# Performance work log

Hardware: AMD Instinct MI355X
Metric: run time of the kernel (lower is better)

## Reference

```python
import jax, jax.numpy as jnp
import numpy as np

B, S, E, H, LD, P, NC = 4, 256, 256, 8, 128, 256, 2
N = S * P  # total points (static)
EPS = 1e-5


def setup_inputs() -> dict:
    key = jax.random.key(0)
    ks = jax.random.split(key, 12)
    r = lambda i, shape, s: jax.random.normal(ks[i], shape, jnp.float32) * s
    return dict(
        gl_feats=jax.random.normal(ks[0], (S, B, E), jnp.float32),
        lo_feats=jax.random.normal(ks[1], (B, N, LD), jnp.float32),
        centroids=jax.random.normal(ks[2], (B, S, 2), jnp.float32),
        np_cluster=jnp.full((S,), P, jnp.int32),
        fc1_w=r(3, (16, 2), 0.5), fc1_b=jnp.zeros(16, jnp.float32),
        fc2_w=r(4, (E, 16), 0.1), fc2_b=jnp.zeros(E, jnp.float32),
        in_proj_w=r(5, (3 * E, E), 0.05), in_proj_b=jnp.zeros(3 * E, jnp.float32),
        out_proj_w=r(6, (E, E), 0.05), out_proj_b=jnp.zeros(E, jnp.float32),
        conv2_w=r(7, (E // 2, LD + E), 0.05), conv2_b=jnp.zeros(E // 2, jnp.float32),
        bn2_gamma=jnp.ones(E // 2, jnp.float32), bn2_beta=jnp.zeros(E // 2, jnp.float32),
        bn2_mean=jnp.zeros(E // 2, jnp.float32), bn2_var=jnp.ones(E // 2, jnp.float32),
        conv3_w=r(8, (64, E // 2), 0.05), conv3_b=jnp.zeros(64, jnp.float32),
        bn3_gamma=jnp.ones(64, jnp.float32), bn3_beta=jnp.zeros(64, jnp.float32),
        bn3_mean=jnp.zeros(64, jnp.float32), bn3_var=jnp.ones(64, jnp.float32),
        conv4_w=r(9, (NC, 64), 0.05), conv4_b=jnp.zeros(NC, jnp.float32),
    )


def _bn(z, g, b, m, v):
    # inference-mode BatchNorm1d over the channel (last) axis
    return (z - m) * jax.lax.rsqrt(v + EPS) * g + b


def reference(gl_feats, lo_feats, centroids, np_cluster,
              fc1_w, fc1_b, fc2_w, fc2_b,
              in_proj_w, in_proj_b, out_proj_w, out_proj_b,
              conv2_w, conv2_b, bn2_gamma, bn2_beta, bn2_mean, bn2_var,
              conv3_w, conv3_b, bn3_gamma, bn3_beta, bn3_mean, bn3_var,
              conv4_w, conv4_b):
    # positional encoding of centroids: Linear(2,16) -> leaky_relu -> Linear(16,E)
    h = centroids @ fc1_w.T + fc1_b                      # [B,S,16]
    h = jnp.where(h >= 0, h, 0.01 * h)                   # leaky_relu_, slope 0.01
    pos = h @ fc2_w.T + fc2_b                            # [B,S,E]
    x = gl_feats.transpose(1, 0, 2) + pos                # [B,S,E] (torch MHA is seq-first)

    # MultiheadAttention (self-attn, eval-mode dropout=identity)
    qkv = x @ in_proj_w.T + in_proj_b                    # [B,S,3E]
    q, k, v = jnp.split(qkv, 3, axis=-1)
    dh = E // H
    qh = q.reshape(B, S, H, dh)
    kh = k.reshape(B, S, H, dh)
    vh = v.reshape(B, S, H, dh)
    scores = jnp.einsum('bqhd,bkhd->bhqk', qh, kh) * (1.0 / np.sqrt(dh))
    attn = jax.nn.softmax(scores, axis=-1)               # [B,H,S,S]
    ctx = jnp.einsum('bhqk,bkhd->bqhd', attn, vh).reshape(B, S, E)
    attn_out = ctx @ out_proj_w.T + out_proj_b           # [B,S,E]

    # segment-broadcast: replace the python repeat/cat loop with a gather
    cluster_ids = jnp.repeat(jnp.arange(S), np_cluster, total_repeat_length=N)  # [N]
    global_feat = attn_out[:, cluster_ids, :]            # [B,N,E]

    pc = jnp.concatenate([lo_feats, global_feat], axis=2)  # [B,N,LD+E]
    # 1x1 Conv1d == pointwise Linear over channels
    h2 = jax.nn.relu(_bn(pc @ conv2_w.T + conv2_b, bn2_gamma, bn2_beta, bn2_mean, bn2_var))
    h3 = jax.nn.relu(_bn(h2 @ conv3_w.T + conv3_b, bn3_gamma, bn3_beta, bn3_mean, bn3_var))
    out = h3 @ conv4_w.T + conv4_b                       # [B,N,NC]
    return out.transpose(0, 2, 1)                        # [B,NC,N] to match torch layout
```

## Files before the change

### kernel.cpp

```cpp
#include <hip/hip_runtime.h>

#define B_   4
#define S_   256
#define E_   256
#define H_   8
#define LD_  128
#define N_   65536
#define NC_  2

typedef __attribute__((ext_vector_type(8))) short s8v;
typedef __attribute__((ext_vector_type(4))) float f32x4;

__device__ __forceinline__ short f2bf(float f) {
  union { float f; unsigned u; } v; v.f = f;
  unsigned r = (v.u + 0x7FFFu + ((v.u >> 16) & 1u)) >> 16;
  return (short)r;
}
__device__ __forceinline__ float bf2f(short s) {
  union { float f; unsigned u; } v; v.u = ((unsigned)(unsigned short)s) << 16;
  return v.f;
}
__device__ __forceinline__ s8v pack8(float4 a, float4 b) {
  s8v r;
  r[0] = f2bf(a.x); r[1] = f2bf(a.y); r[2] = f2bf(a.z); r[3] = f2bf(a.w);
  r[4] = f2bf(b.x); r[5] = f2bf(b.y); r[6] = f2bf(b.z); r[7] = f2bf(b.w);
  return r;
}

__global__ __launch_bounds__(256) void prep_k(
    const int* __restrict__ npc, int* __restrict__ ids,
    const float* __restrict__ ipw, const float* __restrict__ opw,
    const float* __restrict__ w2, const float* __restrict__ w3,
    const float* __restrict__ b2, const float* __restrict__ g2,
    const float* __restrict__ be2, const float* __restrict__ mu2,
    const float* __restrict__ va2,
    const float* __restrict__ b3, const float* __restrict__ g3,
    const float* __restrict__ be3, const float* __restrict__ mu3,
    const float* __restrict__ va3,
    short* __restrict__ iph, short* __restrict__ ipl,
    short* __restrict__ oph, short* __restrict__ opl,
    short* __restrict__ w2bf, short* __restrict__ w3bf,
    float* __restrict__ sc2, float* __restrict__ sh2,
    float* __restrict__ sc3, float* __restrict__ sh3,
    const float* __restrict__ gl, const float* __restrict__ cen,
    const float* __restrict__ fc1w, const float* __restrict__ fc1b,
    const float* __restrict__ fc2w, const float* __restrict__ fc2b,
    short* __restrict__ Xhi, short* __restrict__ Xlo) {
  __shared__ int red[256];
  __shared__ float hsh[16];
  int bid = blockIdx.x, t = threadIdx.x;
  if (bid < 768) {
    int i = bid * 256 + t;
    if (i < 196608) {
      float v = ipw[i]; short h = f2bf(v);
      iph[i] = h; ipl[i] = f2bf(v - bf2f(h));
    }
    if (i < 65536) {
      float v = opw[i]; short h = f2bf(v);
      oph[i] = h; opl[i] = f2bf(v - bf2f(h));
    }
    if (i < 49152) w2bf[i] = f2bf(w2[i]);
    if (i < 8192)  w3bf[i] = f2bf(w3[i]);
    if (i < 128) {
      float sc = g2[i] * rsqrtf(va2[i] + 1e-5f);
      sc2[i] = sc; sh2[i] = (b2[i] - mu2[i]) * sc + be2[i];
    }
    if (i < 64) {
      float sc = g3[i] * rsqrtf(va3[i] + 1e-5f);
      sc3[i] = sc; sh3[i] = (b3[i] - mu3[i]) * sc + be3[i];
    }
  } else if (bid <= 1024) {
    int s = bid - 768;
    int val = (s == 256) ? npc[t] : ((t < s) ? npc[t] : 0);
    red[t] = val;
    __syncthreads();
    for (int off = 128; off > 0; off >>= 1) {
      if (t < off) red[t] += red[t + off];
      __syncthreads();
    }
    int st = red[0];
    if (s < 256) {
      int en = st + npc[s]; if (en > N_) en = N_;
      for (int n = st + t; n < en; n += 256) ids[n] = s;
    } else {
      for (int n = st + t; n < N_; n += 256) ids[n] = 255;
    }
  } else {
    int bs = bid - 1025;
    int b = bs >> 8, s = bs & 255;
    if (t < 16) {
      float c0 = cen[bs * 2 + 0], c1 = cen[bs * 2 + 1];
      float v = c0 * fc1w[2 * t] + c1 * fc1w[2 * t + 1] + fc1b[t];
      hsh[t] = (v >= 0.f) ? v : 0.01f * v;
    }
    __syncthreads();
    float p = fc2b[t];
#pragma unroll
    for (int j = 0; j < 16; j++) p += hsh[j] * fc2w[t * 16 + j];
    float v = gl[((size_t)s * B_ + b) * E_ + t] + p;
    short h = f2bf(v);
    Xhi[(size_t)bs * E_ + t] = h;
    Xlo[(size_t)bs * E_ + t] = f2bf(v - bf2f(h));
  }
}

__global__ __launch_bounds__(256) void gemm_x3_k(
    const short* __restrict__ Ah, const short* __restrict__ Al,
    const short* __restrict__ Wh, const short* __restrict__ Wl,
    const float* __restrict__ bias, float* __restrict__ Cf,
    int M, int N, int K) {
  __shared__ __align__(16) short gs[18432];
  const int AH = 0, AL = 4608, WH = 9216, WL = 13824;
  int t = threadIdx.x;
  int row0 = blockIdx.x * 64, col0 = blockIdx.y * 64;
  int w = t >> 6, l = t & 63, quad = l >> 4, lr = l & 15;
  int m0 = w * 16;
  int ar = t >> 2, aq = (t & 3) * 16;
  f32x4 acc[4];
#pragma unroll
  for (int i = 0; i < 4; i++) acc[i] = (f32x4)(0.f);

  for (int kc = 0; kc < K; kc += 64) {
    __syncthreads();
    {
      size_t ra = (size_t)(row0 + ar) * K + kc + aq;
      size_t rw = (size_t)(col0 + ar) * K + kc + aq;
      *(s8v*)&gs[AH + ar * 72 + aq]     = *(const s8v*)&Ah[ra];
      *(s8v*)&gs[AH + ar * 72 + aq + 8] = *(const s8v*)&Ah[ra + 8];
      *(s8v*)&gs[AL + ar * 72 + aq]     = *(const s8v*)&Al[ra];
      *(s8v*)&gs[AL + ar * 72 + aq + 8] = *(const s8v*)&Al[ra + 8];
      *(s8v*)&gs[WH + ar * 72 + aq]     = *(const s8v*)&Wh[rw];
      *(s8v*)&gs[WH + ar * 72 + aq + 8] = *(const s8v*)&Wh[rw + 8];
      *(s8v*)&gs[WL + ar * 72 + aq]     = *(const s8v*)&Wl[rw];
      *(s8v*)&gs[WL + ar * 72 + aq + 8] = *(const s8v*)&Wl[rw + 8];
    }
    __syncthreads();
#pragma unroll
    for (int ks = 0; ks < 2; ks++) {
      int ko = ks * 32 + quad * 8;
      s8v ah = *(const s8v*)&gs[AH + (m0 + lr) * 72 + ko];
      s8v al = *(const s8v*)&gs[AL + (m0 + lr) * 72 + ko];
#pragma unroll
      for (int ct = 0; ct < 4; ct++) {
        s8v bh = *(const s8v*)&gs[WH + (ct * 16 + lr) * 72 + ko];
        s8v bl = *(const s8v*)&gs[WL + (ct * 16 + lr) * 72 + ko];
        acc[ct] = __builtin_amdgcn_mfma_f32_16x16x32_bf16(ah, bh, acc[ct], 0, 0, 0);
        acc[ct] = __builtin_amdgcn_mfma_f32_16x16x32_bf16(al, bh, acc[ct], 0, 0, 0);
        acc[ct] = __builtin_amdgcn_mfma_f32_16x16x32_bf16(ah, bl, acc[ct], 0, 0, 0);
      }
    }
  }
#pragma unroll
  for (int ct = 0; ct < 4; ct++) {
    int c = col0 + ct * 16 + lr;
    float bb = bias[c];
#pragma unroll
    for (int rg = 0; rg < 4; rg++) {
      int r = row0 + m0 + quad * 4 + rg;
      Cf[(size_t)r * N + c] = acc[ct][rg] + bb;
    }
  }
}

__global__ __launch_bounds__(256) void attn_k(const float* __restrict__ qkv,
                                              short* __restrict__ Chi,
                                              short* __restrict__ Clo) {
  int bid = blockIdx.x;
  int qt = bid & 7, h = (bid >> 3) & 7, b = bid >> 6;
  __shared__ __align__(16) float smem[16384];
  float* Kx = smem;
  float* Vx = smem + 8192;
  int t = threadIdx.x;
#pragma unroll
  for (int i = 0; i < 8; i++) {
    int row = i * 32 + (t >> 3);
    int d4 = (t & 7) * 4;
    const float* base = qkv + (size_t)(b * S_ + row) * 768 + h * 32 + d4;
    *(float4*)&Kx[row * 32 + d4] = *(const float4*)(base + 256);
    *(float4*)&Vx[row * 32 + d4] = *(const float4*)(base + 512);
  }
  int r = t & 31, g = t >> 5;
  float q[32];
  {
    const float* qb = qkv + (size_t)(b * S_ + qt * 32 + r) * 768 + h * 32;
#pragma unroll
    for (int d4 = 0; d4 < 32; d4 += 4) {
      float4 v = *(const float4*)(qb + d4);
      q[d4] = v.x; q[d4 + 1] = v.y; q[d4 + 2] = v.z; q[d4 + 3] = v.w;
    }
  }
  __syncthreads();
  const float scale = 0.17677669529663687f;
  int kk0 = g * 32;
  float sc[32];
  float m = -1e30f;
#pragma unroll
  for (int kk = 0; kk < 32; kk++) {
    const float* kr = &Kx[(kk0 + kk) * 32];
    float4 a = (float4){0.f, 0.f, 0.f, 0.f};
#pragma unroll
    for (int d4 = 0; d4 < 32; d4 += 4) {
      float4 kv = *(const float4*)(kr + d4);
      a.x += q[d4] * kv.x; a.y += q[d4 + 1] * kv.y;
      a.z += q[d4 + 2] * kv.z; a.w += q[d4 + 3] * kv.w;
    }
    float s = ((a.x + a.y) + (a.z + a.w)) * scale;
    sc[kk] = s;
    m = fmaxf(m, s);
  }
  float lsum = 0.f;
  float ctx[32];
#pragma unroll
  for (int d = 0; d < 32; d++) ctx[d] = 0.f;
#pragma unroll
  for (int kk = 0; kk < 32; kk++) {
    const float* vr = &Vx[(kk0 + kk) * 32];
    float p = __expf(sc[kk] - m);
    lsum += p;
#pragma unroll
    for (int d4 = 0; d4 < 32; d4 += 4) {
      float4 vv = *(const float4*)(vr + d4);
      ctx[d4] += p * vv.x; ctx[d4 + 1] += p * vv.y;
      ctx[d4 + 2] += p * vv.z; ctx[d4 + 3] += p * vv.w;
    }
  }
  __syncthreads();
  float* ctxbuf = smem;
  float* mbuf = smem + 8192;
  float* lbuf = smem + 8448;
  mbuf[g * 32 + r] = m;
  lbuf[g * 32 + r] = lsum;
#pragma unroll
  for (int d = 0; d < 32; d++)
    ctxbuf[(g * 32 + r) * 32 + ((d + r) & 31)] = ctx[d];
  __syncthreads();
  int r2 = t & 31, dq = t >> 5;
  float M = -1e30f;
#pragma unroll
  for (int gg = 0; gg < 8; gg++) M = fmaxf(M, mbuf[gg * 32 + r2]);
  float wg[8]; float L = 0.f;
#pragma unroll
  for (int gg = 0; gg < 8; gg++) {
    wg[gg] = __expf(mbuf[gg * 32 + r2] - M);
    L += lbuf[gg * 32 + r2] * wg[gg];
  }
  float invL = 1.f / L;
  size_t base = (size_t)(b * S_ + qt * 32 + r2) * E_ + h * 32;
#pragma unroll
  for (int dd = 0; dd < 4; dd++) {
    int d = dq * 4 + dd;
    float o = 0.f;
#pragma unroll
    for (int gg = 0; gg < 8; gg++)
      o += ctxbuf[(gg * 32 + r2) * 32 + ((d + r2) & 31)] * wg[gg];
    o *= invL;
    short hi = f2bf(o);
    Chi[base + d] = hi;
    Clo[base + d] = f2bf(o - bf2f(hi));
  }
}

__global__ __launch_bounds__(256) void opg_k(
    const short* __restrict__ Chi, const short* __restrict__ Clo,
    const short* __restrict__ oph, const short* __restrict__ opl,
    const float* __restrict__ opb, const short* __restrict__ w2bf,
    float* __restrict__ G) {
  __shared__ __align__(16) short gsm[50688];
  const int AH = 0, AL = 4608, WH = 9216, WL = 27648;
  const int CT = 0, W2B = 16896;
  int t = threadIdx.x;
  int row0 = blockIdx.x * 64;
  int w = t >> 6, l = t & 63, quad = l >> 4, lr = l & 15;

  f32x4 acc[16];
#pragma unroll
  for (int i = 0; i < 16; i++) acc[i] = (f32x4)(0.f);

  for (int kc = 0; kc < 256; kc += 64) {
    __syncthreads();
    {
#pragma unroll
      for (int j = 0; j < 8; j++) {
        *(s8v*)&gsm[WH + t * 72 + j * 8] = *(const s8v*)&oph[(size_t)t * 256 + kc + j * 8];
        *(s8v*)&gsm[WL + t * 72 + j * 8] = *(const s8v*)&opl[(size_t)t * 256 + kc + j * 8];
      }
      if (t < 128) {
        int row = t >> 1, half = (t & 1) * 32;
        size_t ra = (size_t)(row0 + row) * 256 + kc + half;
#pragma unroll
        for (int j = 0; j < 4; j++) {
          *(s8v*)&gsm[AH + row * 72 + half + j * 8] = *(const s8v*)&Chi[ra + j * 8];
          *(s8v*)&gsm[AL + row * 72 + half + j * 8] = *(const s8v*)&Clo[ra + j * 8];
        }
      }
    }
    __syncthreads();
#pragma unroll
    for (int ks = 0; ks < 2; ks++) {
      int ko = ks * 32 + quad * 8;
      s8v ah = *(const s8v*)&gsm[AH + (w * 16 + lr) * 72 + ko];
      s8v al = *(const s8v*)&gsm[AL + (w * 16 + lr) * 72 + ko];
#pragma unroll
      for (int ct = 0; ct < 16; ct++) {
        s8v bh = *(const s8v*)&gsm[WH + (ct * 16 + lr) * 72 + ko];
        s8v bl = *(const s8v*)&gsm[WL + (ct * 16 + lr) * 72 + ko];
        acc[ct] = __builtin_amdgcn_mfma_f32_16x16x32_bf16(ah, bh, acc[ct], 0, 0, 0);
        acc[ct] = __builtin_amdgcn_mfma_f32_16x16x32_bf16(al, bh, acc[ct], 0, 0, 0);
        acc[ct] = __builtin_amdgcn_mfma_f32_16x16x32_bf16(ah, bl, acc[ct], 0, 0, 0);
      }
    }
  }
  __syncthreads();
#pragma unroll
  for (int ct = 0; ct < 16; ct++) {
    int c = ct * 16 + lr;
    float bb = opb[c];
#pragma unroll
    for (int rg = 0; rg < 4; rg++) {
      int r = w * 16 + quad * 4 + rg;
      gsm[CT + r * 264 + c] = f2bf(acc[ct][rg] + bb);
    }
  }
  {
    int ch = t >> 1, koff = (t & 1) * 128;
#pragma unroll
    for (int j = 0; j < 16; j++)
      *(s8v*)&gsm[W2B + ch * 264 + koff + j * 8] =
          *(const s8v*)&w2bf[(size_t)ch * 384 + 128 + koff + j * 8];
  }
  __syncthreads();
  f32x4 acc2[8];
#pragma unroll
  for (int i = 0; i < 8; i++) acc2[i] = (f32x4)(0.f);
#pragma unroll
  for (int ks = 0; ks < 8; ks++) {
    int ko = ks * 32 + quad * 8;
    s8v a = *(const s8v*)&gsm[CT + (w * 16 + lr) * 264 + ko];
#pragma unroll
    for (int ct = 0; ct < 8; ct++) {
      s8v b = *(const s8v*)&gsm[W2B + (ct * 16 + lr) * 264 + ko];
      acc2[ct] = __builtin_amdgcn_mfma_f32_16x16x32_bf16(a, b, acc2[ct], 0, 0, 0);
    }
  }
#pragma unroll
  for (int ct = 0; ct < 8; ct++) {
    int c = ct * 16 + lr;
#pragma unroll
    for (int rg = 0; rg < 4; rg++) {
      int r = row0 + w * 16 + quad * 4 + rg;
      G[(size_t)r * 128 + c] = acc2[ct][rg];
    }
  }
}

#define CF_SW2 0
#define CF_SA  17408
#define CF_H2  0
#define CF_SW3 17408
#define CF_H3  0

__global__ __launch_bounds__(256, 3) void conv_fused_k(
    const float* __restrict__ lo, const float* __restrict__ G,
    const int* __restrict__ ids,
    const short* __restrict__ w2bf, const short* __restrict__ w3bf,
    const float* __restrict__ sc2, const float* __restrict__ sh2,
    const float* __restrict__ sc3, const float* __restrict__ sh3,
    const float* __restrict__ w4, const float* __restrict__ b4,
    float* __restrict__ out) {
  __shared__ __align__(16) short smem[26624];
  __shared__ int lds_ids[128];
  int t = threadIdx.x;
  int bid = blockIdx.x;
  int b = bid >> 9;
  int n0 = (bid & 511) << 7;
  int w = t >> 6, l = t & 63;
  int quad = l >> 4, lr = l & 15;
  int mh = w & 1, chh = w >> 1;
  int ar = t >> 1, akh = (t & 1) * 32;
  const float* lob = &lo[((size_t)b * N_ + n0 + ar) * LD_ + akh];

  {
    int ch = t >> 1, koff = (t & 1) * 64;
#pragma unroll
    for (int j = 0; j < 8; j++)
      *(s8v*)&smem[CF_SW2 + ch * 136 + koff + j * 8] =
          *(const s8v*)&w2bf[(size_t)ch * 384 + koff + j * 8];
  }
  if (t < 128) lds_ids[t] = ids[n0 + t];
  float4 pf[8];
#pragma unroll
  for (int j = 0; j < 8; j++) pf[j] = *(const float4*)(lob + j * 4);
#pragma unroll
  for (int j = 0; j < 4; j++)
    *(s8v*)&smem[CF_SA + ar * 72 + akh + j * 8] = pack8(pf[2 * j], pf[2 * j + 1]);
  __syncthreads();

#pragma unroll
  for (int j = 0; j < 8; j++) pf[j] = *(const float4*)(lob + 64 + j * 4);

  f32x4 acc2[4][4];
#pragma unroll
  for (int i = 0; i < 4; i++)
#pragma unroll
    for (int j = 0; j < 4; j++) acc2[i][j] = (f32x4)(0.f);

#pragma unroll
  for (int ks = 0; ks < 2; ks++) {
    int ko = ks * 32 + quad * 8;
    s8v af[4], bf[4];
#pragma unroll
    for (int mt = 0; mt < 4; mt++)
      af[mt] = *(const s8v*)&smem[CF_SA + (64 * mh + 16 * mt + lr) * 72 + ko];
#pragma unroll
    for (int ct = 0; ct < 4; ct++)
      bf[ct] = *(const s8v*)&smem[CF_SW2 + (64 * chh + 16 * ct + lr) * 136 + ko];
#pragma unroll
    for (int mt = 0; mt < 4; mt++)
#pragma unroll
      for (int ct = 0; ct < 4; ct++)
        acc2[mt][ct] = __builtin_amdgcn_mfma_f32_16x16x32_bf16(af[mt], bf[ct], acc2[mt][ct], 0, 0, 0);
  }
  __syncthreads();
#pragma unroll
  for (int j = 0; j < 4; j++)
    *(s8v*)&smem[CF_SA + ar * 72 + akh + j * 8] = pack8(pf[2 * j], pf[2 * j + 1]);
  __syncthreads();
#pragma unroll
  for (int ks = 0; ks < 2; ks++) {
    int koA = ks * 32 + quad * 8;
    int koW = 64 + koA;
    s8v af[4], bf[4];
#pragma unroll
    for (int mt = 0; mt < 4; mt++)
      af[mt] = *(const s8v*)&smem[CF_SA + (64 * mh + 16 * mt + lr) * 72 + koA];
#pragma unroll
    for (int ct = 0; ct < 4; ct++)
      bf[ct] = *(const s8v*)&smem[CF_SW2 + (64 * chh + 16 * ct + lr) * 136 + koW];
#pragma unroll
    for (int mt = 0; mt < 4; mt++)
#pragma unroll
      for (int ct = 0; ct < 4; ct++)
        acc2[mt][ct] = __builtin_amdgcn_mfma_f32_16x16x32_bf16(af[mt], bf[ct], acc2[mt][ct], 0, 0, 0);
  }
  __syncthreads();

#pragma unroll
  for (int ct = 0; ct < 4; ct++) {
    int c = 64 * chh + 16 * ct + lr;
    float sc = sc2[c], sh = sh2[c];
    float gv[4][4];
#pragma unroll
    for (int mt = 0; mt < 4; mt++)
#pragma unroll
      for (int rg = 0; rg < 4; rg++) {
        int p = 64 * mh + 16 * mt + 4 * quad + rg;
        gv[mt][rg] = G[((size_t)b * 256 + lds_ids[p]) * 128 + c];
      }
#pragma unroll
    for (int mt = 0; mt < 4; mt++)
#pragma unroll
      for (int rg = 0; rg < 4; rg++) {
        int p = 64 * mh + 16 * mt + 4 * quad + rg;
        float z = (acc2[mt][ct][rg] + gv[mt][rg]) * sc + sh;
        smem[CF_H2 + p * 136 + c] = f2bf(fmaxf(z, 0.f));
      }
  }
  {
    int ch = t >> 2, kq = (t & 3) * 32;
#pragma unroll
    for (int j = 0; j < 4; j++)
      *(s8v*)&smem[CF_SW3 + ch * 136 + kq + j * 8] =
          *(const s8v*)&w3bf[ch * 128 + kq + j * 8];
  }
  __syncthreads();

  f32x4 acc3[2][4];
#pragma unroll
  for (int i = 0; i < 2; i++)
#pragma unroll
    for (int j = 0; j < 4; j++) acc3[i][j] = (f32x4)(0.f);
#pragma unroll
  for (int ks = 0; ks < 4; ks++) {
    int ko = ks * 32 + quad * 8;
    s8v af[2], bf[4];
#pragma unroll
    for (int mt = 0; mt < 2; mt++)
      af[mt] = *(const s8v*)&smem[CF_H2 + (32 * w + 16 * mt + lr) * 136 + ko];
#pragma unroll
    for (int ct = 0; ct < 4; ct++)
      bf[ct] = *(const s8v*)&smem[CF_SW3 + (16 * ct + lr) * 136 + ko];
#pragma unroll
    for (int mt = 0; mt < 2; mt++)
#pragma unroll
      for (int ct = 0; ct < 4; ct++)
        acc3[mt][ct] = __builtin_amdgcn_mfma_f32_16x16x32_bf16(af[mt], bf[ct], acc3[mt][ct], 0, 0, 0);
  }
  __syncthreads();

#pragma unroll
  for (int ct = 0; ct < 4; ct++) {
    int c = 16 * ct + lr;
    float sc = sc3[c], sh = sh3[c];
#pragma unroll
    for (int mt = 0; mt < 2; mt++)
#pragma unroll
      for (int rg = 0; rg < 4; rg++) {
        int p = 32 * w + 16 * mt + 4 * quad + rg;
        float z = acc3[mt][ct][rg] * sc + sh;
        smem[CF_H3 + p * 72 + c] = f2bf(fmaxf(z, 0.f));
      }
  }
  __syncthreads();

  {
    int c = t >> 7, p = t & 127;
    float s = b4[c];
#pragma unroll
    for (int j = 0; j < 8; j++) {
      s8v hv = *(const s8v*)&smem[CF_H3 + p * 72 + j * 8];
#pragma unroll
      for (int e = 0; e < 8; e++)
        s += bf2f(hv[e]) * w4[c * 64 + j * 8 + e];
    }
    out[((size_t)b * NC_ + c) * N_ + n0 + p] = s;
  }
}

extern "C" void kernel_launch(void* const* d_in, const int* in_sizes, int n_in,
                              void* d_out, int out_size, void* d_ws, size_t ws_size,
                              hipStream_t stream) {
  const float* gl   = (const float*)d_in[0];
  const float* lo   = (const float*)d_in[1];
  const float* cen  = (const float*)d_in[2];
  const int*   npc  = (const int*)d_in[3];
  const float* fc1w = (const float*)d_in[4];
  const float* fc1b = (const float*)d_in[5];
  const float* fc2w = (const float*)d_in[6];
  const float* fc2b = (const float*)d_in[7];
  const float* ipw  = (const float*)d_in[8];
  const float* ipb  = (const float*)d_in[9];
  const float* opw  = (const float*)d_in[10];
  const float* opb  = (const float*)d_in[11];
  const float* w2   = (const float*)d_in[12];
  const float* b2   = (const float*)d_in[13];
  const float* g2   = (const float*)d_in[14];
  const float* be2  = (const float*)d_in[15];
  const float* mu2  = (const float*)d_in[16];
  const float* va2  = (const float*)d_in[17];
  const float* w3   = (const float*)d_in[18];
  const float* b3   = (const float*)d_in[19];
  const float* g3   = (const float*)d_in[20];
  const float* be3  = (const float*)d_in[21];
  const float* mu3  = (const float*)d_in[22];
  const float* va3  = (const float*)d_in[23];
  const float* w4   = (const float*)d_in[24];
  const float* b4   = (const float*)d_in[25];

  char* ws = (char*)d_ws;
  float* qkv  = (float*)(ws);
  short* Xhi  = (short*)(ws + 3145728);
  short* Xlo  = (short*)(ws + 3670016);
  short* Chi  = (short*)(ws + 4194304);
  short* Clo  = (short*)(ws + 4718592);
  float* G    = (float*)(ws + 5242880);
  short* iph  = (short*)(ws + 5767168);
  short* ipl  = (short*)(ws + 6160384);
  short* oph  = (short*)(ws + 6553600);
  short* opl  = (short*)(ws + 6684672);
  short* w2bf = (short*)(ws + 6815744);
  short* w3bf = (short*)(ws + 6914048);
  int*   ids  = (int*)  (ws + 6930432);
  float* sc2  = (float*)(ws + 7192576);
  float* sh2  = (float*)(ws + 7193088);
  float* sc3  = (float*)(ws + 7193600);
  float* sh3  = (float*)(ws + 7193856);
  float* out  = (float*)d_out;

  prep_k<<<2049, 256, 0, stream>>>(npc, ids, ipw, opw, w2, w3,
                                   b2, g2, be2, mu2, va2,
                                   b3, g3, be3, mu3, va3,
                                   iph, ipl, oph, opl, w2bf, w3bf,
                                   sc2, sh2, sc3, sh3,
                                   gl, cen, fc1w, fc1b, fc2w, fc2b, Xhi, Xlo);
  gemm_x3_k<<<dim3(16, 12), 256, 0, stream>>>(Xhi, Xlo, iph, ipl, ipb,
                                              qkv, B_ * S_, 768, E_);
  attn_k<<<B_ * H_ * 8, 256, 0, stream>>>(qkv, Chi, Clo);
  opg_k<<<16, 256, 0, stream>>>(Chi, Clo, oph, opl, opb, w2bf, G);
  conv_fused_k<<<B_ * (N_ / 128), 256, 0, stream>>>(
      lo, G, ids, w2bf, w3bf, sc2, sh2, sc3, sh3, w4, b4, out);
}
```

Before: 310.4 us.

## Shrink LDS in conv kernel and split out-proj GEMM across more blocks

The out-proj/G kernel now uses 16-row tiles with each wave owning a column slice, so it launches 64 blocks instead of 16 and spreads the small GEMM over more CUs. The fused conv kernel stages the W2 slice per K chunk alongside the activation chunk, reads W3 fragments directly from global memory instead of staging them in LDS, and shrinks shared memory so that launch bounds can allow 4 blocks per CU. This trades more global and L2 traffic for the weights, and drops the register prefetch of the second lo chunk, in exchange for higher occupancy.

Result: no change. 313.2 us (+0.9%).

```diff
diff --git a/kernel.cpp b/kernel.cpp
--- a/kernel.cpp
+++ b/kernel.cpp
@@ -265,16 +265,16 @@
     const short* __restrict__ oph, const short* __restrict__ opl,
     const float* __restrict__ opb, const short* __restrict__ w2bf,
     float* __restrict__ G) {
-  __shared__ __align__(16) short gsm[50688];
-  const int AH = 0, AL = 4608, WH = 9216, WL = 27648;
-  const int CT = 0, W2B = 16896;
+  __shared__ __align__(16) short gsm[39168];
+  const int AH = 0, AL = 1152, WH = 2304, WL = 20736;
+  const int CT = 0, W2B = 4352;
   int t = threadIdx.x;
-  int row0 = blockIdx.x * 64;
+  int row0 = blockIdx.x * 16;
   int w = t >> 6, l = t & 63, quad = l >> 4, lr = l & 15;
 
-  f32x4 acc[16];
-#pragma unroll
-  for (int i = 0; i < 16; i++) acc[i] = (f32x4)(0.f);
+  f32x4 acc[4];
+#pragma unroll
+  for (int i = 0; i < 4; i++) acc[i] = (f32x4)(0.f);
 
   for (int kc = 0; kc < 256; kc += 64) {
     __syncthreads();
@@ -284,7 +284,7 @@
         *(s8v*)&gsm[WH + t * 72 + j * 8] = *(const s8v*)&oph[(size_t)t * 256 + kc + j * 8];
         *(s8v*)&gsm[WL + t * 72 + j * 8] = *(const s8v*)&opl[(size_t)t * 256 + kc + j * 8];
       }
-      if (t < 128) {
+      if (t < 32) {
         int row = t >> 1, half = (t & 1) * 32;
         size_t ra = (size_t)(row0 + row) * 256 + kc + half;
 #pragma unroll
@@ -298,12 +298,12 @@
 #pragma unroll
     for (int ks = 0; ks < 2; ks++) {
       int ko = ks * 32 + quad * 8;
-      s8v ah = *(const s8v*)&gsm[AH + (w * 16 + lr) * 72 + ko];
-      s8v al = *(const s8v*)&gsm[AL + (w * 16 + lr) * 72 + ko];
-#pragma unroll
-      for (int ct = 0; ct < 16; ct++) {
-        s8v bh = *(const s8v*)&gsm[WH + (ct * 16 + lr) * 72 + ko];
-        s8v bl = *(const s8v*)&gsm[WL + (ct * 16 + lr) * 72 + ko];
+      s8v ah = *(const s8v*)&gsm[AH + lr * 72 + ko];
+      s8v al = *(const s8v*)&gsm[AL + lr * 72 + ko];
+#pragma unroll
+      for (int ct = 0; ct < 4; ct++) {
+        s8v bh = *(const s8v*)&gsm[WH + (w * 64 + ct * 16 + lr) * 72 + ko];
+        s8v bl = *(const s8v*)&gsm[WL + (w * 64 + ct * 16 + lr) * 72 + ko];
         acc[ct] = __builtin_amdgcn_mfma_f32_16x16x32_bf16(ah, bh, acc[ct], 0, 0, 0);
         acc[ct] = __builtin_amdgcn_mfma_f32_16x16x32_bf16(al, bh, acc[ct], 0, 0, 0);
         acc[ct] = __builtin_amdgcn_mfma_f32_16x16x32_bf16(ah, bl, acc[ct], 0, 0, 0);
@@ -312,12 +312,12 @@
   }
   __syncthreads();
 #pragma unroll
-  for (int ct = 0; ct < 16; ct++) {
-    int c = ct * 16 + lr;
+  for (int ct = 0; ct < 4; ct++) {
+    int c = w * 64 + ct * 16 + lr;
     float bb = opb[c];
 #pragma unroll
     for (int rg = 0; rg < 4; rg++) {
-      int r = w * 16 + quad * 4 + rg;
+      int r = quad * 4 + rg;
       gsm[CT + r * 264 + c] = f2bf(acc[ct][rg] + bb);
     }
   }
@@ -329,37 +329,36 @@
           *(const s8v*)&w2bf[(size_t)ch * 384 + 128 + koff + j * 8];
   }
   __syncthreads();
-  f32x4 acc2[8];
-#pragma unroll
-  for (int i = 0; i < 8; i++) acc2[i] = (f32x4)(0.f);
+  f32x4 acc2[2];
+#pragma unroll
+  for (int i = 0; i < 2; i++) acc2[i] = (f32x4)(0.f);
 #pragma unroll
   for (int ks = 0; ks < 8; ks++) {
     int ko = ks * 32 + quad * 8;
-    s8v a = *(const s8v*)&gsm[CT + (w * 16 + lr) * 264 + ko];
-#pragma unroll
-    for (int ct = 0; ct < 8; ct++) {
-      s8v b = *(const s8v*)&gsm[W2B + (ct * 16 + lr) * 264 + ko];
-      acc2[ct] = __builtin_amdgcn_mfma_f32_16x16x32_bf16(a, b, acc2[ct], 0, 0, 0);
-    }
-  }
-#pragma unroll
-  for (int ct = 0; ct < 8; ct++) {
-    int c = ct * 16 + lr;
+    s8v a = *(const s8v*)&gsm[CT + lr * 264 + ko];
+#pragma unroll
+    for (int cc = 0; cc < 2; cc++) {
+      s8v b = *(const s8v*)&gsm[W2B + (w * 32 + cc * 16 + lr) * 264 + ko];
+      acc2[cc] = __builtin_amdgcn_mfma_f32_16x16x32_bf16(a, b, acc2[cc], 0, 0, 0);
+    }
+  }
+#pragma unroll
+  for (int cc = 0; cc < 2; cc++) {
+    int c = w * 32 + cc * 16 + lr;
 #pragma unroll
     for (int rg = 0; rg < 4; rg++) {
-      int r = row0 + w * 16 + quad * 4 + rg;
-      G[(size_t)r * 128 + c] = acc2[ct][rg];
-    }
-  }
-}
-
-#define CF_SW2 0
-#define CF_SA  17408
-#define CF_H2  0
-#define CF_SW3 17408
-#define CF_H3  0
-
-__global__ __launch_bounds__(256, 3) void conv_fused_k(
+      int r = row0 + quad * 4 + rg;
+      G[(size_t)r * 128 + c] = acc2[cc][rg];
+    }
+  }
+}
+
+#define CV_SA  0
+#define CV_SW  9216
+#define CV_H2  0
+#define CV_H3  0
+
+__global__ __launch_bounds__(256, 4) void conv_fused_k(
     const float* __restrict__ lo, const float* __restrict__ G,
     const int* __restrict__ ids,
     const short* __restrict__ w2bf, const short* __restrict__ w3bf,
@@ -367,7 +366,7 @@
     const float* __restrict__ sc3, const float* __restrict__ sh3,
     const float* __restrict__ w4, const float* __restrict__ b4,
     float* __restrict__ out) {
-  __shared__ __align__(16) short smem[26624];
+  __shared__ __align__(16) short smem[18432];
   __shared__ int lds_ids[128];
   int t = threadIdx.x;
   int bid = blockIdx.x;
@@ -378,25 +377,9 @@
   int mh = w & 1, chh = w >> 1;
   int ar = t >> 1, akh = (t & 1) * 32;
   const float* lob = &lo[((size_t)b * N_ + n0 + ar) * LD_ + akh];
-
-  {
-    int ch = t >> 1, koff = (t & 1) * 64;
-#pragma unroll
-    for (int j = 0; j < 8; j++)
-      *(s8v*)&smem[CF_SW2 + ch * 136 + koff + j * 8] =
-          *(const s8v*)&w2bf[(size_t)ch * 384 + koff + j * 8];
-  }
+  const short* wb  = &w2bf[(size_t)ar * 384 + akh];
+
   if (t < 128) lds_ids[t] = ids[n0 + t];
-  float4 pf[8];
-#pragma unroll
-  for (int j = 0; j < 8; j++) pf[j] = *(const float4*)(lob + j * 4);
-#pragma unroll
-  for (int j = 0; j < 4; j++)
-    *(s8v*)&smem[CF_SA + ar * 72 + akh + j * 8] = pack8(pf[2 * j], pf[2 * j + 1]);
-  __syncthreads();
-
-#pragma unroll
-  for (int j = 0; j < 8; j++) pf[j] = *(const float4*)(lob + 64 + j * 4);
 
   f32x4 acc2[4][4];
 #pragma unroll
@@ -404,43 +387,37 @@
 #pragma unroll
     for (int j = 0; j < 4; j++) acc2[i][j] = (f32x4)(0.f);
 
-#pragma unroll
-  for (int ks = 0; ks < 2; ks++) {
-    int ko = ks * 32 + quad * 8;
-    s8v af[4], bf[4];
-#pragma unroll
-    for (int mt = 0; mt < 4; mt++)
-      af[mt] = *(const s8v*)&smem[CF_SA + (64 * mh + 16 * mt + lr) * 72 + ko];
-#pragma unroll
-    for (int ct = 0; ct < 4; ct++)
-      bf[ct] = *(const s8v*)&smem[CF_SW2 + (64 * chh + 16 * ct + lr) * 136 + ko];
-#pragma unroll
-    for (int mt = 0; mt < 4; mt++)
+  for (int kc = 0; kc < 2; kc++) {
+    if (kc) __syncthreads();
+    {
+      float4 v0, v1;
+#pragma unroll
+      for (int j = 0; j < 4; j++) {
+        v0 = *(const float4*)(lob + kc * 64 + j * 8);
+        v1 = *(const float4*)(lob + kc * 64 + j * 8 + 4);
+        *(s8v*)&smem[CV_SA + ar * 72 + akh + j * 8] = pack8(v0, v1);
+      }
+#pragma unroll
+      for (int j = 0; j < 4; j++)
+        *(s8v*)&smem[CV_SW + ar * 72 + akh + j * 8] = *(const s8v*)(wb + kc * 64 + j * 8);
+    }
+    __syncthreads();
+#pragma unroll
+    for (int ks = 0; ks < 2; ks++) {
+      int ko = ks * 32 + quad * 8;
+      s8v af[4], bf[4];
+#pragma unroll
+      for (int mt = 0; mt < 4; mt++)
+        af[mt] = *(const s8v*)&smem[CV_SA + (64 * mh + 16 * mt + lr) * 72 + ko];
 #pragma unroll
       for (int ct = 0; ct < 4; ct++)
-        acc2[mt][ct] = __builtin_amdgcn_mfma_f32_16x16x32_bf16(af[mt], bf[ct], acc2[mt][ct], 0, 0, 0);
-  }
-  __syncthreads();
-#pragma unroll
-  for (int j = 0; j < 4; j++)
-    *(s8v*)&smem[CF_SA + ar * 72 + akh + j * 8] = pack8(pf[2 * j], pf[2 * j + 1]);
-  __syncthreads();
-#pragma unroll
-  for (int ks = 0; ks < 2; ks++) {
-    int koA = ks * 32 + quad * 8;
-    int koW = 64 + koA;
-    s8v af[4], bf[4];
-#pragma unroll
-    for (int mt = 0; mt < 4; mt++)
-      af[mt] = *(const s8v*)&smem[CF_SA + (64 * mh + 16 * mt + lr) * 72 + koA];
-#pragma unroll
-    for (int ct = 0; ct < 4; ct++)
-      bf[ct] = *(const s8v*)&smem[CF_SW2 + (64 * chh + 16 * ct + lr) * 136 + koW];
-#pragma unroll
-    for (int mt = 0; mt < 4; mt++)
-#pragma unroll
-      for (int ct = 0; ct < 4; ct++)
-        acc2[mt][ct] = __builtin_amdgcn_mfma_f32_16x16x32_bf16(af[mt], bf[ct], acc2[mt][ct], 0, 0, 0);
+        bf[ct] = *(const s8v*)&smem[CV_SW + (64 * chh + 16 * ct + lr) * 72 + ko];
+#pragma unroll
+      for (int mt = 0; mt < 4; mt++)
+#pragma unroll
+        for (int ct = 0; ct < 4; ct++)
+          acc2[mt][ct] = __builtin_amdgcn_mfma_f32_16x16x32_bf16(af[mt], bf[ct], acc2[mt][ct], 0, 0, 0);
+    }
   }
   __syncthreads();
 
@@ -448,29 +425,21 @@
   for (int ct = 0; ct < 4; ct++) {
     int c = 64 * chh + 16 * ct + lr;
     float sc = sc2[c], sh = sh2[c];
-    float gv[4][4];
-#pragma unroll
-    for (int mt = 0; mt < 4; mt++)
+#pragma unroll
+    for (int mt = 0; mt < 4; mt++) {
+      float gv[4];
 #pragma unroll
       for (int rg = 0; rg < 4; rg++) {
         int p = 64 * mh + 16 * mt + 4 * quad + rg;
-        gv[mt][rg] = G[((size_t)b * 256 + lds_ids[p]) * 128 + c];
-      }
-#pragma unroll
-    for (int mt = 0; mt < 4; mt++)
+        gv[rg] = G[((size_t)b * 256 + lds_ids[p]) * 128 + c];
+      }
 #pragma unroll
       for (int rg = 0; rg < 4; rg++) {
         int p = 64 * mh + 16 * mt + 4 * quad + rg;
-        float z = (acc2[mt][ct][rg] + gv[mt][rg]) * sc + sh;
-        smem[CF_H2 + p * 136 + c] = f2bf(fmaxf(z, 0.f));
-      }
-  }
-  {
-    int ch = t >> 2, kq = (t & 3) * 32;
-#pragma unroll
-    for (int j = 0; j < 4; j++)
-      *(s8v*)&smem[CF_SW3 + ch * 136 + kq + j * 8] =
-          *(const s8v*)&w3bf[ch * 128 + kq + j * 8];
+        float z = (acc2[mt][ct][rg] + gv[rg]) * sc + sh;
+        smem[CV_H2 + p * 136 + c] = f2bf(fmaxf(z, 0.f));
+      }
+    }
   }
   __syncthreads();
 
@@ -485,10 +454,10 @@
     s8v af[2], bf[4];
 #pragma unroll
     for (int mt = 0; mt < 2; mt++)
-      af[mt] = *(const s8v*)&smem[CF_H2 + (32 * w + 16 * mt + lr) * 136 + ko];
+      af[mt] = *(const s8v*)&smem[CV_H2 + (32 * w + 16 * mt + lr) * 136 + ko];
 #pragma unroll
     for (int ct = 0; ct < 4; ct++)
-      bf[ct] = *(const s8v*)&smem[CF_SW3 + (16 * ct + lr) * 136 + ko];
+      bf[ct] = *(const s8v*)&w3bf[(size_t)(16 * ct + lr) * 128 + ko];
 #pragma unroll
     for (int mt = 0; mt < 2; mt++)
 #pragma unroll
@@ -507,7 +476,7 @@
       for (int rg = 0; rg < 4; rg++) {
         int p = 32 * w + 16 * mt + 4 * quad + rg;
         float z = acc3[mt][ct][rg] * sc + sh;
-        smem[CF_H3 + p * 72 + c] = f2bf(fmaxf(z, 0.f));
+        smem[CV_H3 + p * 72 + c] = f2bf(fmaxf(z, 0.f));
       }
   }
   __syncthreads();
@@ -517,7 +486,7 @@
     float s = b4[c];
 #pragma unroll
     for (int j = 0; j < 8; j++) {
-      s8v hv = *(const s8v*)&smem[CF_H3 + p * 72 + j * 8];
+      s8v hv = *(const s8v*)&smem[CV_H3 + p * 72 + j * 8];
 #pragma unroll
       for (int e = 0; e < 8; e++)
         s += bf2f(hv[e]) * w4[c * 64 + j * 8 + e];
@@ -585,7 +554,7 @@
   gemm_x3_k<<<dim3(16, 12), 256, 0, stream>>>(Xhi, Xlo, iph, ipl, ipb,
                                               qkv, B_ * S_, 768, E_);
   attn_k<<<B_ * H_ * 8, 256, 0, stream>>>(qkv, Chi, Clo);
-  opg_k<<<16, 256, 0, stream>>>(Chi, Clo, oph, opl, opb, w2bf, G);
+  opg_k<<<64, 256, 0, stream>>>(Chi, Clo, oph, opl, opb, w2bf, G);
   conv_fused_k<<<B_ * (N_ / 128), 256, 0, stream>>>(
       lo, G, ids, w2bf, w3bf, sc2, sh2, sc3, sh3, w4, b4, out);
 }
```
